# Optimization experiments

Hardware: AMD Instinct MI355X
Metric: run time of the kernel (lower is better)

Reference implementation:

```python
import jax, jax.numpy as jnp
import numpy as np

STRIDES = (8, 16, 32)
SIZES = ((80, 80), (40, 40), (20, 20))  # 640x640 input
PRE_TOP_K = 1000
KEEP_TOP_K = 100
IOU_THR = 0.65
SCORE_THR = 0.25
CLASS_OFFSET = 4096.0  # > max image extent, for class-aware NMS


def setup_inputs() -> dict:
    key = jax.random.key(0)
    ks = jax.random.split(key, 6)
    B, C = 8, 1203
    d = {}
    for i, (h, w) in enumerate(SIZES):
        d[f"cls_scores_{i}"] = jax.random.normal(ks[i], (B, C, h, w), dtype=jnp.float32)
        d[f"bbox_preds_{i}"] = jax.random.uniform(ks[3 + i], (B, 4, h, w), dtype=jnp.float32)
    return d


def _flatten(feats, ch):
    B = feats[0].shape[0]
    return jnp.concatenate([f.transpose(0, 2, 3, 1).reshape(B, -1, ch) for f in feats], axis=1)


def _priors():
    pts, strs = [], []
    for (h, w), s in zip(SIZES, STRIDES):
        yy, xx = jnp.meshgrid(jnp.arange(h, dtype=jnp.float32), jnp.arange(w, dtype=jnp.float32), indexing="ij")
        pts.append(jnp.stack([(xx.ravel() + 0.5) * s, (yy.ravel() + 0.5) * s], axis=-1))
        strs.append(jnp.full((h * w,), float(s), dtype=jnp.float32))
    return jnp.concatenate(pts, 0), jnp.concatenate(strs, 0)


def _decode(priors, preds, stride):
    # DistancePointBBoxCoder: preds are LTRB distances scaled by stride.
    d = preds * stride[None, :, None]  # [B,N,4]
    x1 = priors[None, :, 0] - d[..., 0]
    y1 = priors[None, :, 1] - d[..., 1]
    x2 = priors[None, :, 0] + d[..., 2]
    y2 = priors[None, :, 1] + d[..., 3]
    return jnp.stack([x1, y1, x2, y2], axis=-1)


def _iou_matrix(b):
    area = (b[:, 2] - b[:, 0]) * (b[:, 3] - b[:, 1])
    lt = jnp.maximum(b[:, None, :2], b[None, :, :2])
    rb = jnp.minimum(b[:, None, 2:], b[None, :, 2:])
    wh = jnp.clip(rb - lt, 0.0)
    inter = wh[..., 0] * wh[..., 1]
    return inter / (area[:, None] + area[None, :] - inter + 1e-7)


def _nms_single(boxes, scores, labels):
    # boxes [N,4], scores [N] (max over classes), labels [N] int
    ts, idx = jax.lax.top_k(scores, PRE_TOP_K)
    b = boxes[idx]
    l = labels[idx]
    valid = ts > SCORE_THR
    off = b + (l.astype(b.dtype) * CLASS_OFFSET)[:, None]  # class-aware trick
    iou = _iou_matrix(off)  # [K,K]

    def body(keep, i):
        suppressed = jnp.any(keep & (iou[:, i] > IOU_THR))
        keep = keep.at[i].set(valid[i] & ~suppressed)
        return keep, None

    keep, _ = jax.lax.scan(body, jnp.zeros((PRE_TOP_K,), bool), jnp.arange(PRE_TOP_K))
    kept_scores = jnp.where(keep, ts, -1.0)
    fs, fi = jax.lax.top_k(kept_scores, KEEP_TOP_K)
    m = fs > 0.0
    det_boxes = jnp.where(m[:, None], b[fi], 0.0)
    det_scores = jnp.where(m, fs, 0.0)
    det_labels = jnp.where(m, l[fi], -1)
    num_dets = m.sum().astype(jnp.int32)
    return num_dets, det_boxes, det_scores, det_labels


def reference(cls_scores_0, cls_scores_1, cls_scores_2, bbox_preds_0, bbox_preds_1, bbox_preds_2):
    C = cls_scores_0.shape[1]
    cls_scores = jax.nn.sigmoid(_flatten([cls_scores_0, cls_scores_1, cls_scores_2], C))  # [B,N,C]
    preds = _flatten([bbox_preds_0, bbox_preds_1, bbox_preds_2], 4)  # [B,N,4]
    priors, stride = _priors()
    boxes = _decode(priors, preds, stride)  # [B,N,4]
    max_scores = cls_scores.max(axis=-1)  # [B,N]
    labels = cls_scores.argmax(axis=-1)  # [B,N]
    num_dets, det_boxes, det_scores, det_labels = jax.vmap(_nms_single)(boxes, max_scores, labels)
    return num_dets, det_boxes, det_scores, det_labels
```

## Files before the change

kernel.cpp:

```cpp
#include <hip/hip_runtime.h>
#include <math.h>

#pragma clang fp contract(off)

typedef unsigned long long u64;
typedef unsigned int u32;
typedef float f4 __attribute__((ext_vector_type(4)));
typedef unsigned long long u64x2 __attribute__((ext_vector_type(2)));

#define BB 8
#define CC_TOT 1203
#define NANC 8400
#define NSEL 1000
#define NCAND 1024
#define NT 1024
#define NBATCH 128
#define NCHUNK_MAX 16

__device__ __forceinline__ u32 okey32(float v) {
  u32 b = __float_as_uint(v);
  return (b & 0x80000000u) ? ~b : (b | 0x80000000u);
}

__device__ __forceinline__ float unokey32(u32 ok) {
  u32 fb = (ok & 0x80000000u) ? (ok & 0x7FFFFFFFu) : ~ok;
  return __uint_as_float(fb);
}

__global__ __launch_bounds__(256) void kmax(const float* __restrict__ cls0,
                                            const float* __restrict__ cls1,
                                            const float* __restrict__ cls2,
                                            u64* __restrict__ part,
                                            int chunkSz, int nchunk) {
  int bx = blockIdx.x;
  int per = nchunk * BB;
  int tg = bx / per;
  int rem = bx - tg * per;
  int chunk = rem >> 3;
  int b = rem & 7;
  const float* cls; int hw4, aoff, col0;
  if (tg < 7)      { cls = cls0; hw4 = 1600; aoff = 0;    col0 = tg << 8; }
  else if (tg < 9) { cls = cls1; hw4 = 400;  aoff = 6400; col0 = (tg - 7) << 8; }
  else             { cls = cls2; hw4 = 100;  aoff = 8000; col0 = 0; }
  int col = col0 + (int)threadIdx.x;
  if (col >= hw4) return;
  int c0 = chunk * chunkSz;
  int c1 = c0 + chunkSz; if (c1 > CC_TOT) c1 = CC_TOT;

  const f4* base = (const f4*)cls + (size_t)b * CC_TOT * hw4 + col;
  f4 m = (f4){-3.4e38f, -3.4e38f, -3.4e38f, -3.4e38f};
  int ix0 = c0, ix1 = c0, ix2 = c0, ix3 = c0;

#define UPD(v, c)                                   \
  do {                                              \
    if ((v)[0] > m[0]) { m[0] = (v)[0]; ix0 = (c); } \
    if ((v)[1] > m[1]) { m[1] = (v)[1]; ix1 = (c); } \
    if ((v)[2] > m[2]) { m[2] = (v)[2]; ix2 = (c); } \
    if ((v)[3] > m[3]) { m[3] = (v)[3]; ix3 = (c); } \
  } while (0)

  int c = c0;
  for (; c + 8 <= c1; c += 8) {
    const f4* p = base + (size_t)c * hw4;
    f4 v0 = p[0];
    f4 v1 = p[(size_t)1 * hw4];
    f4 v2 = p[(size_t)2 * hw4];
    f4 v3 = p[(size_t)3 * hw4];
    f4 v4 = p[(size_t)4 * hw4];
    f4 v5 = p[(size_t)5 * hw4];
    f4 v6 = p[(size_t)6 * hw4];
    f4 v7 = p[(size_t)7 * hw4];
    UPD(v0, c + 0); UPD(v1, c + 1); UPD(v2, c + 2); UPD(v3, c + 3);
    UPD(v4, c + 4); UPD(v5, c + 5); UPD(v6, c + 6); UPD(v7, c + 7);
  }
  for (; c < c1; ++c) {
    f4 v = base[(size_t)c * hw4];
    UPD(v, c);
  }
#undef UPD

  u64* dst = part + ((size_t)chunk * BB + b) * NANC + aoff + (size_t)col * 4;
  u64x2 s01 = { ((u64)okey32(m[0]) << 32) | (u64)(u32)~(u32)ix0,
                ((u64)okey32(m[1]) << 32) | (u64)(u32)~(u32)ix1 };
  u64x2 s23 = { ((u64)okey32(m[2]) << 32) | (u64)(u32)~(u32)ix2,
                ((u64)okey32(m[3]) << 32) | (u64)(u32)~(u32)ix3 };
  *((u64x2*)dst)     = s01;
  *((u64x2*)dst + 1) = s23;
}

__global__ __launch_bounds__(256) void kreduce(const u64* __restrict__ part,
                                               u64* __restrict__ fin, int nchunk) {
  int a = blockIdx.x * 256 + threadIdx.x;
  if (a >= NANC) return;
  int b = blockIdx.y;
  size_t off = (size_t)b * NANC + a;
  const size_t PL = (size_t)BB * NANC;
  const u64* p = part + off;
  u64 m = p[0];
  int ch = 1;
  for (; ch + 4 <= nchunk; ch += 4) {
    u64 v0 = p[(size_t)(ch + 0) * PL];
    u64 v1 = p[(size_t)(ch + 1) * PL];
    u64 v2 = p[(size_t)(ch + 2) * PL];
    u64 v3 = p[(size_t)(ch + 3) * PL];
    u64 a01 = (v0 > v1) ? v0 : v1;
    u64 a23 = (v2 > v3) ? v2 : v3;
    u64 a03 = (a01 > a23) ? a01 : a23;
    m = (a03 > m) ? a03 : m;
  }
  for (; ch < nchunk; ++ch) {
    u64 v = p[(size_t)ch * PL];
    m = (v > m) ? v : m;
  }
  u32 lab = ~(u32)m;
  fin[off] = (m & 0xFFFFFFFF00000000ull) | ((u64)(u32)(0xFFFFu - (u32)a) << 16) | (u64)(lab & 0xFFFFu);
}

struct DecodeArrays {
  float xo1[NCAND], yo1[NCAND], xo2[NCAND], yo2[NCAND], ar[NCAND];
  float rx1[NCAND], ry1[NCAND], rx2[NCAND], ry2[NCAND], sc[NCAND];
  int lab[NCAND], val[NCAND];
};

__device__ __forceinline__ void hist_add_clustered(u32* hist, u32 digit, int lane) {
  u64 peers = ~0ull;
  for (int bit = 0; bit < 13; ++bit) {
    u64 bal = __ballot((digit >> bit) & 1u);
    peers &= ((digit >> bit) & 1u) ? bal : ~bal;
  }
  int leader = __ffsll((unsigned long long)peers) - 1;
  if (digit < 4096u && lane == leader)
    atomicAdd(&hist[digit], (u32)__popcll((unsigned long long)peers));
}

__device__ __forceinline__ void suffix_pick(u32* hist, u32* waveTot, u32* waveSufExcl,
                                            u64* prefixSh, u32* rankSh,
                                            u64 prefix, u32 rank, int shift,
                                            int tid, int lane, int wv) {
  u32 l0 = hist[4 * tid], l1 = hist[4 * tid + 1], l2 = hist[4 * tid + 2], l3 = hist[4 * tid + 3];
  u32 psum = l0 + l1 + l2 + l3;
  u32 x = psum;
  for (int s = 1; s < 64; s <<= 1) { u32 v = __shfl_down(x, s); if (lane + s < 64) x += v; }
  if (lane == 0) waveTot[wv] = x;
  __syncthreads();
  if (tid < 16) {
    u32 y = waveTot[tid]; u32 z = y;
    for (int s = 1; s < 16; s <<= 1) { u32 v = __shfl_down(z, s); if (tid + s < 16) z += v; }
    waveSufExcl[tid] = z - y;
  }
  __syncthreads();
  u32 S = x + waveSufExcl[wv];
  u32 G3 = S - psum; u32 G2 = G3 + l3; u32 G1 = G2 + l2; u32 G0 = G1 + l1;
  u32 r = rank;
  if      (G3 < r && G3 + l3 >= r) { *prefixSh = prefix | ((u64)(4u * tid + 3) << shift); *rankSh = r - G3; }
  else if (G2 < r && G2 + l2 >= r) { *prefixSh = prefix | ((u64)(4u * tid + 2) << shift); *rankSh = r - G2; }
  else if (G1 < r && G1 + l1 >= r) { *prefixSh = prefix | ((u64)(4u * tid + 1) << shift); *rankSh = r - G1; }
  else if (G0 < r && G0 + l0 >= r) { *prefixSh = prefix | ((u64)(4u * tid + 0) << shift); *rankSh = r - G0; }
}

__device__ __forceinline__ u64 radix_select(const u64* keys, int n, u32 target,
                                            u32* hist, u32* waveTot, u32* waveSufExcl,
                                            u64* prefixSh, u32* rankSh,
                                            int tid, int lane, int wv) {
  u64 prefix = 0; u32 rank = target;
  for (int pass = 3; pass >= 0; --pass) {
    int shift = 16 + pass * 12;
    for (int i = tid; i < 4096; i += NT) hist[i] = 0;
    __syncthreads();
    u64 hiMask = (pass == 3) ? 0ull : ((~0ull) << (shift + 12));
    if (pass == 3) {
      for (int i = tid; i < n; i += NT) {
        u64 k = keys[i];
        hist_add_clustered(hist, (u32)((k >> shift) & 4095u), lane);
      }
    } else {
      for (int i = tid; i < n; i += NT) {
        u64 k = keys[i];
        if ((k & hiMask) == (prefix & hiMask))
          atomicAdd(&hist[(u32)((k >> shift) & 4095u)], 1u);
      }
    }
    __syncthreads();
    suffix_pick(hist, waveTot, waveSufExcl, prefixSh, rankSh, prefix, rank, shift, tid, lane, wv);
    __syncthreads();
    prefix = *prefixSh; rank = *rankSh;
    __syncthreads();
  }
  return prefix;
}

__device__ __forceinline__ void gather_ge(const u64* keys, int n, u64 K, u64* dst, u32* cnt,
                                          int tid, int lane, u32 bound) {
  for (int i = tid; i < n; i += NT) {
    u64 k = keys[i];
    bool sel = (k >= K);
    u64 mask = __ballot(sel);
    if (mask) {
      int leader = __ffsll((unsigned long long)mask) - 1;
      u32 basep = 0;
      if (lane == leader) basep = atomicAdd(cnt, (u32)__popcll((unsigned long long)mask));
      basep = __shfl((int)basep, leader);
      if (sel) {
        u32 pos = basep + (u32)__popcll((unsigned long long)(mask & ((1ull << lane) - 1ull)));
        if (pos < bound) dst[pos] = k;
      }
    }
  }
}

__device__ __forceinline__ void decode_into(DecodeArrays* d, int rk, u64 my, int b,
                                            const float* bb0, const float* bb1, const float* bb2) {
  int label = (int)(u32)(my & 0xFFFFull);
  int idx = 0xFFFF - (int)(u32)((my >> 16) & 0xFFFFull);
  float logit = unokey32((u32)(my >> 32));
  float sc = 1.0f / (1.0f + expf(-logit));

  int w, str, off, hwl; const float* bb;
  if (idx < 6400)      { w = 80; str = 8;  off = 0;    hwl = 6400; bb = bb0; }
  else if (idx < 8000) { w = 40; str = 16; off = 6400; hwl = 1600; bb = bb1; }
  else                 { w = 20; str = 32; off = 8000; hwl = 400;  bb = bb2; }
  int p = idx - off;
  int y = p / w;
  int x = p - y * w;
  float fs = (float)str;
  float px = ((float)x + 0.5f) * fs;
  float py = ((float)y + 0.5f) * fs;
  const float* bp = bb + (size_t)b * 4 * hwl + p;
  float t0 = bp[0] * fs;
  float t1 = bp[hwl] * fs;
  float t2 = bp[2 * hwl] * fs;
  float t3 = bp[3 * hwl] * fs;
  float x1 = px - t0, y1 = py - t1, x2 = px + t2, y2 = py + t3;
  float lo = (float)label * 4096.0f;
  float ox1 = x1 + lo, oy1 = y1 + lo, ox2 = x2 + lo, oy2 = y2 + lo;
  float area = (ox2 - ox1) * (oy2 - oy1);

  d->xo1[rk] = ox1; d->yo1[rk] = oy1; d->xo2[rk] = ox2; d->yo2[rk] = oy2; d->ar[rk] = area;
  d->rx1[rk] = x1;  d->ry1[rk] = y1;  d->rx2[rk] = x2;  d->ry2[rk] = y2;  d->sc[rk] = sc;
  d->lab[rk] = label;
  d->val[rk] = (sc > 0.25f) ? 1 : 0;
}

__device__ __forceinline__ int nms_pass(const DecodeArrays* d, int bound, int lane, int* outIdx) {
  float ax1 = 0, ay1 = 0, ax2 = 0, ay2 = 0, aar = 0; int aon = 0;
  float bx1 = 0, by1 = 0, bx2 = 0, by2 = 0, bar = 0; int bon = 0;
  int kept = 0;
  for (int i = 0; i < bound; ++i) {
    if (kept >= 100) break;
    float cx1 = d->xo1[i], cy1 = d->yo1[i], cx2 = d->xo2[i], cy2 = d->yo2[i], car = d->ar[i];
    bool sup = false;
    if (aon) {
      float ltx = fmaxf(ax1, cx1), lty = fmaxf(ay1, cy1);
      float rbx = fminf(ax2, cx2), rby = fminf(ay2, cy2);
      float wd = fmaxf(rbx - ltx, 0.0f), ht = fmaxf(rby - lty, 0.0f);
      float inter = wd * ht;
      sup = sup || ((inter / (aar + car - inter + 1e-7f)) > 0.65f);
    }
    if (bon) {
      float ltx = fmaxf(bx1, cx1), lty = fmaxf(by1, cy1);
      float rbx = fminf(bx2, cx2), rby = fminf(by2, cy2);
      float wd = fmaxf(rbx - ltx, 0.0f), ht = fmaxf(rby - lty, 0.0f);
      float inter = wd * ht;
      sup = sup || ((inter / (bar + car - inter + 1e-7f)) > 0.65f);
    }
    bool anysup = __any(sup);
    if (d->val[i] != 0 && !anysup) {
      if (kept < 64) {
        if (lane == kept) { ax1 = cx1; ay1 = cy1; ax2 = cx2; ay2 = cy2; aar = car; aon = 1; }
      } else {
        if (lane == kept - 64) { bx1 = cx1; by1 = cy1; bx2 = cx2; by2 = cy2; bar = car; bon = 1; }
      }
      if (lane == 0) outIdx[kept] = i;
      ++kept;
    }
  }
  return kept;
}

__global__ __launch_bounds__(1024) void knms(const u64* __restrict__ fin,
                                             const float* __restrict__ bb0,
                                             const float* __restrict__ bb1,
                                             const float* __restrict__ bb2,
                                             float* __restrict__ out) {
  __shared__ union ShU {
    u64 fk[NANC];
    DecodeArrays d;
  } sh;
  __shared__ u32 hist[4096];
  __shared__ u32 waveTot[16];
  __shared__ u32 waveSufExcl[16];
  __shared__ u64 prefixSh;
  __shared__ u32 rankSh;
  __shared__ u32 gcnt, aCnt, cCnt;
  __shared__ __align__(16) u64 cand[NCAND];
  __shared__ __align__(16) u64 candA[NBATCH];
  __shared__ __align__(16) u32 cm[NBATCH * 4];
  __shared__ u64 VwSh[2];
  __shared__ int outIdx[128];
  __shared__ int keptSh;

  int b = blockIdx.x;
  int tid = threadIdx.x;
  int lane = tid & 63;
  int wv = tid >> 6;

  for (int i = tid; i < 4096; i += NT) hist[i] = 0;
  if (tid == 0) { aCnt = 0; cCnt = 0; }
  __syncthreads();
  {
    const u64x2* fsrc = (const u64x2*)(fin + (size_t)b * NANC);
    u64x2* fdst = (u64x2*)sh.fk;
    for (int i = tid; i < NANC / 2; i += NT) {
      u64x2 v = fsrc[i];
      fdst[i] = v;
      hist_add_clustered(hist, (u32)(v[0] >> 52), lane);
      hist_add_clustered(hist, (u32)(v[1] >> 52), lane);
    }
  }
  __syncthreads();

  suffix_pick(hist, waveTot, waveSufExcl, &prefixSh, &rankSh, 0ull, NBATCH, 52, tid, lane, wv);
  __syncthreads();
  u64 pfx3 = prefixSh; u32 r3 = rankSh;
  u32 d3 = (u32)(pfx3 >> 52);
  __syncthreads();

  for (int i = tid; i < NANC; i += NT) {
    u64 k = sh.fk[i];
    u32 dig = (u32)(k >> 52);
    bool selA = dig > d3;
    u64 mA = __ballot(selA);
    if (mA) {
      int leader = __ffsll((unsigned long long)mA) - 1;
      u32 basep = 0;
      if (lane == leader) basep = atomicAdd(&aCnt, (u32)__popcll((unsigned long long)mA));
      basep = __shfl((int)basep, leader);
      if (selA) {
        u32 pos = basep + (u32)__popcll((unsigned long long)(mA & ((1ull << lane) - 1ull)));
        if (pos < NBATCH) candA[pos] = k;
      }
    }
    bool selC = (dig == d3);
    u64 mC = __ballot(selC);
    if (mC) {
      int leader = __ffsll((unsigned long long)mC) - 1;
      u32 basep = 0;
      if (lane == leader) basep = atomicAdd(&cCnt, (u32)__popcll((unsigned long long)mC));
      basep = __shfl((int)basep, leader);
      if (selC) {
        u32 pos = basep + (u32)__popcll((unsigned long long)(mC & ((1ull << lane) - 1ull)));
        if (pos < NCAND) cand[pos] = k;
      }
    }
  }
  __syncthreads();

  u32 cnt3 = cCnt;
  if (cnt3 <= NCAND) {
    u64 pfx = pfx3; u32 rk = r3;
    for (int pass = 2; pass >= 0; --pass) {
      int shift = 16 + pass * 12;
      for (int i = tid; i < 4096; i += NT) hist[i] = 0;
      __syncthreads();
      u64 hiMask = (~0ull) << (shift + 12);
      for (int i = tid; i < (int)cnt3; i += NT) {
        u64 k = cand[i];
        if ((k & hiMask) == (pfx & hiMask))
          atomicAdd(&hist[(u32)((k >> shift) & 4095u)], 1u);
      }
      __syncthreads();
      suffix_pick(hist, waveTot, waveSufExcl, &prefixSh, &rankSh, pfx, rk, shift, tid, lane, wv);
      __syncthreads();
      pfx = prefixSh; rk = rankSh;
      __syncthreads();
    }
    u64 K2 = pfx;
    gather_ge(cand, (int)cnt3, K2, candA, &aCnt, tid, lane, NBATCH);
    __syncthreads();
  } else {
    if (tid == 0) aCnt = 0;
    __syncthreads();
    u64 K2 = radix_select(sh.fk, NANC, NBATCH, hist, waveTot, waveSufExcl,
                          &prefixSh, &rankSh, tid, lane, wv);
    gather_ge(sh.fk, NANC, K2, candA, &aCnt, tid, lane, NBATCH);
    __syncthreads();
  }

  if (tid < NBATCH) {
    u64 my = candA[tid];
    int rk = 0;
    const u64x2* cav = (const u64x2*)candA;
    #pragma unroll
    for (int j2 = 0; j2 < NBATCH / 2; ++j2) {
      u64x2 p = cav[j2];
      rk += (p[0] > my) ? 1 : 0;
      rk += (p[1] > my) ? 1 : 0;
    }
    decode_into(&sh.d, rk, my, b, bb0, bb1, bb2);
  }
  if (tid < NBATCH * 4) cm[tid] = 0;
  __syncthreads();

  if (tid < NBATCH) {
    u64 bal = __ballot(sh.d.val[tid] != 0);
    if (lane == 0) VwSh[tid >> 6] = bal;
  }

  {
    int c = tid & 127;
    int g = tid >> 7;
    float cx1 = sh.d.xo1[c], cy1 = sh.d.yo1[c], cx2 = sh.d.xo2[c], cy2 = sh.d.yo2[c], car = sh.d.ar[c];
    u32 bits = 0;
    int j0 = g * 16;
    for (int jj = 0; jj < 16; ++jj) {
      int j = j0 + jj;
      float ltx = fmaxf(sh.d.xo1[j], cx1), lty = fmaxf(sh.d.yo1[j], cy1);
      float rbx = fminf(sh.d.xo2[j], cx2), rby = fminf(sh.d.yo2[j], cy2);
      float wd = fmaxf(rbx - ltx, 0.0f), ht = fmaxf(rby - lty, 0.0f);
      float inter = wd * ht;
      bool sup = (inter / (sh.d.ar[j] + car - inter + 1e-7f)) > 0.65f;
      bits |= sup ? (1u << jj) : 0u;
    }
    atomicOr(&cm[c * 4 + (g >> 1)], bits << ((g & 1) * 16));
  }
  __syncthreads();

  if (tid == 0) {
    u32 K0 = 0, K1 = 0, K2w = 0, K3 = 0;
    u64 V0 = VwSh[0], V1 = VwSh[1];
    int kept = 0;
    for (int i = 0; i < NBATCH && kept < 100; ++i) {
      const u32* c4 = &cm[i * 4];
      u32 sup = (c4[0] & K0) | (c4[1] & K1) | (c4[2] & K2w) | (c4[3] & K3);
      bool valid = (((i < 64) ? (V0 >> i) : (V1 >> (i - 64))) & 1ull) != 0ull;
      if (valid && sup == 0u) {
        if (i < 32) K0 |= 1u << i;
        else if (i < 64) K1 |= 1u << (i - 32);
        else if (i < 96) K2w |= 1u << (i - 64);
        else K3 |= 1u << (i - 96);
        outIdx[kept++] = i;
      }
    }
    keptSh = kept;
  }
  __syncthreads();

  if (keptSh < 100) {
    {
      const u64x2* fsrc = (const u64x2*)(fin + (size_t)b * NANC);
      u64x2* fdst = (u64x2*)sh.fk;
      for (int i = tid; i < NANC / 2; i += NT) fdst[i] = fsrc[i];
    }
    __syncthreads();
    u64 K = radix_select(sh.fk, NANC, NSEL, hist, waveTot, waveSufExcl,
                         &prefixSh, &rankSh, tid, lane, wv);
    if (tid == 0) gcnt = 0;
    __syncthreads();
    gather_ge(sh.fk, NANC, K, cand, &gcnt, tid, lane, NSEL);
    __syncthreads();
    if (tid < NSEL) {
      u64 my = cand[tid];
      int rk = 0;
      const u64x2* cbv = (const u64x2*)cand;
      for (int j2 = 0; j2 < NSEL / 2; ++j2) {
        u64x2 p = cbv[j2];
        rk += (p[0] > my) ? 1 : 0;
        rk += (p[1] > my) ? 1 : 0;
      }
      decode_into(&sh.d, rk, my, b, bb0, bb1, bb2);
    }
    __syncthreads();
    if (tid < 64) {
      int kept = nms_pass(&sh.d, NSEL, lane, outIdx);
      if (lane == 0) keptSh = kept;
    }
    __syncthreads();
  }

  int kept = keptSh;
  float* o_nd = out;
  float* o_box = out + BB;
  float* o_sc = out + BB + BB * 100 * 4;
  float* o_lb = out + BB + BB * 100 * 4 + BB * 100;
  if (tid == 0) o_nd[b] = (float)kept;
  if (tid < 100) {
    int s = tid;
    float v0 = 0, v1 = 0, v2 = 0, v3 = 0, sv = 0, lv = -1.0f;
    if (s < kept) {
      int i = outIdx[s];
      v0 = sh.d.rx1[i]; v1 = sh.d.ry1[i]; v2 = sh.d.rx2[i]; v3 = sh.d.ry2[i];
      sv = sh.d.sc[i]; lv = (float)sh.d.lab[i];
    }
    float* bo = o_box + ((size_t)b * 100 + s) * 4;
    bo[0] = v0; bo[1] = v1; bo[2] = v2; bo[3] = v3;
    o_sc[b * 100 + s] = sv;
    o_lb[b * 100 + s] = lv;
  }
}

extern "C" void kernel_launch(void* const* d_in, const int* in_sizes, int n_in,
                              void* d_out, int out_size, void* d_ws, size_t ws_size,
                              hipStream_t stream) {
  const float* cls0 = (const float*)d_in[0];
  const float* bb0  = (const float*)d_in[1];
  const float* cls1 = (const float*)d_in[2];
  const float* bb1  = (const float*)d_in[3];
  const float* cls2 = (const float*)d_in[4];
  const float* bb2  = (const float*)d_in[5];

  size_t planeB = (size_t)BB * NANC * sizeof(u64);
  u64* fin = (u64*)d_ws;
  u64* part;
  int nchunk;
  if (ws_size >= 2 * planeB) {
    size_t avail = (ws_size - planeB) / planeB;
    nchunk = (int)(avail < NCHUNK_MAX ? avail : NCHUNK_MAX);
    part = fin + (size_t)BB * NANC;
  } else {
    nchunk = 1;
    part = fin;
  }
  int chunkSz = (CC_TOT + nchunk - 1) / nchunk;
  nchunk = (CC_TOT + chunkSz - 1) / chunkSz;

  kmax<<<dim3(10 * nchunk * BB), dim3(256), 0, stream>>>(cls0, cls1, cls2, part, chunkSz, nchunk);
  kreduce<<<dim3((NANC + 255) / 256, BB), dim3(256), 0, stream>>>(part, fin, nchunk);
  knms<<<dim3(BB), dim3(NT), 0, stream>>>(fin, bb0, bb1, bb2, (float*)d_out);
}
```

Before: 120.7 us.

## Fuse chunk reduction into NMS kernel and shortcut radix selection

Removes the separate kreduce launch and has the NMS kernel reduce the per-chunk partial max keys directly while building the first histogram. This drops one kernel launch and the round trip through the fin buffer. It also adds an early exit from the radix select when the chosen bin holds exactly the remaining rank, and replaces the greedy 128-candidate keep loop with a find-first-set walk over a live mask. The cost is that only 8 blocks now do the chunk reduction, and they do it again in the fallback path.

```diff
diff --git a/kernel.cpp b/kernel.cpp
--- a/kernel.cpp
+++ b/kernel.cpp
@@ -88,40 +88,37 @@
   *((u64x2*)dst + 1) = s23;
 }
 
-__global__ __launch_bounds__(256) void kreduce(const u64* __restrict__ part,
-                                               u64* __restrict__ fin, int nchunk) {
-  int a = blockIdx.x * 256 + threadIdx.x;
-  if (a >= NANC) return;
-  int b = blockIdx.y;
-  size_t off = (size_t)b * NANC + a;
-  const size_t PL = (size_t)BB * NANC;
-  const u64* p = part + off;
-  u64 m = p[0];
-  int ch = 1;
-  for (; ch + 4 <= nchunk; ch += 4) {
-    u64 v0 = p[(size_t)(ch + 0) * PL];
-    u64 v1 = p[(size_t)(ch + 1) * PL];
-    u64 v2 = p[(size_t)(ch + 2) * PL];
-    u64 v3 = p[(size_t)(ch + 3) * PL];
-    u64 a01 = (v0 > v1) ? v0 : v1;
-    u64 a23 = (v2 > v3) ? v2 : v3;
-    u64 a03 = (a01 > a23) ? a01 : a23;
-    m = (a03 > m) ? a03 : m;
-  }
-  for (; ch < nchunk; ++ch) {
-    u64 v = p[(size_t)ch * PL];
-    m = (v > m) ? v : m;
-  }
-  u32 lab = ~(u32)m;
-  fin[off] = (m & 0xFFFFFFFF00000000ull) | ((u64)(u32)(0xFFFFu - (u32)a) << 16) | (u64)(lab & 0xFFFFu);
-}
-
 struct DecodeArrays {
   float xo1[NCAND], yo1[NCAND], xo2[NCAND], yo2[NCAND], ar[NCAND];
   float rx1[NCAND], ry1[NCAND], rx2[NCAND], ry2[NCAND], sc[NCAND];
   int lab[NCAND], val[NCAND];
 };
 
+__device__ __forceinline__ u64x2 reduce_pair(const u64x2* psrc, size_t PL2, int nchunk, int i) {
+  u64x2 m = psrc[i];
+  for (int ch = 1; ch < nchunk; ++ch) {
+    u64x2 v = psrc[(size_t)ch * PL2 + i];
+    if (v[0] > m[0]) m[0] = v[0];
+    if (v[1] > m[1]) m[1] = v[1];
+  }
+  u32 i0 = (u32)(2 * i), i1 = (u32)(2 * i + 1);
+  u64x2 r;
+  r[0] = (m[0] & 0xFFFFFFFF00000000ull) | ((u64)(0xFFFFu - i0) << 16) | (u64)(~(u32)m[0] & 0xFFFFu);
+  r[1] = (m[1] & 0xFFFFFFFF00000000ull) | ((u64)(0xFFFFu - i1) << 16) | (u64)(~(u32)m[1] & 0xFFFFu);
+  return r;
+}
+
+__device__ __forceinline__ void hist_add12(u32* hist, u32 digit, int lane) {
+  u64 peers = ~0ull;
+  for (int bit = 0; bit < 12; ++bit) {
+    u64 bal = __ballot((digit >> bit) & 1u);
+    peers &= ((digit >> bit) & 1u) ? bal : ~bal;
+  }
+  int leader = __ffsll((unsigned long long)peers) - 1;
+  if (lane == leader)
+    atomicAdd(&hist[digit], (u32)__popcll((unsigned long long)peers));
+}
+
 __device__ __forceinline__ void hist_add_clustered(u32* hist, u32 digit, int lane) {
   u64 peers = ~0ull;
   for (int bit = 0; bit < 13; ++bit) {
@@ -134,7 +131,7 @@
 }
 
 __device__ __forceinline__ void suffix_pick(u32* hist, u32* waveTot, u32* waveSufExcl,
-                                            u64* prefixSh, u32* rankSh,
+                                            u64* prefixSh, u32* rankSh, u32* binCntSh,
                                             u64 prefix, u32 rank, int shift,
                                             int tid, int lane, int wv) {
   u32 l0 = hist[4 * tid], l1 = hist[4 * tid + 1], l2 = hist[4 * tid + 2], l3 = hist[4 * tid + 3];
@@ -152,15 +149,15 @@
   u32 S = x + waveSufExcl[wv];
   u32 G3 = S - psum; u32 G2 = G3 + l3; u32 G1 = G2 + l2; u32 G0 = G1 + l1;
   u32 r = rank;
-  if      (G3 < r && G3 + l3 >= r) { *prefixSh = prefix | ((u64)(4u * tid + 3) << shift); *rankSh = r - G3; }
-  else if (G2 < r && G2 + l2 >= r) { *prefixSh = prefix | ((u64)(4u * tid + 2) << shift); *rankSh = r - G2; }
-  else if (G1 < r && G1 + l1 >= r) { *prefixSh = prefix | ((u64)(4u * tid + 1) << shift); *rankSh = r - G1; }
-  else if (G0 < r && G0 + l0 >= r) { *prefixSh = prefix | ((u64)(4u * tid + 0) << shift); *rankSh = r - G0; }
+  if      (G3 < r && G3 + l3 >= r) { *prefixSh = prefix | ((u64)(4u * tid + 3) << shift); *rankSh = r - G3; *binCntSh = l3; }
+  else if (G2 < r && G2 + l2 >= r) { *prefixSh = prefix | ((u64)(4u * tid + 2) << shift); *rankSh = r - G2; *binCntSh = l2; }
+  else if (G1 < r && G1 + l1 >= r) { *prefixSh = prefix | ((u64)(4u * tid + 1) << shift); *rankSh = r - G1; *binCntSh = l1; }
+  else if (G0 < r && G0 + l0 >= r) { *prefixSh = prefix | ((u64)(4u * tid + 0) << shift); *rankSh = r - G0; *binCntSh = l0; }
 }
 
 __device__ __forceinline__ u64 radix_select(const u64* keys, int n, u32 target,
                                             u32* hist, u32* waveTot, u32* waveSufExcl,
-                                            u64* prefixSh, u32* rankSh,
+                                            u64* prefixSh, u32* rankSh, u32* binCntSh,
                                             int tid, int lane, int wv) {
   u64 prefix = 0; u32 rank = target;
   for (int pass = 3; pass >= 0; --pass) {
@@ -181,7 +178,7 @@
       }
     }
     __syncthreads();
-    suffix_pick(hist, waveTot, waveSufExcl, prefixSh, rankSh, prefix, rank, shift, tid, lane, wv);
+    suffix_pick(hist, waveTot, waveSufExcl, prefixSh, rankSh, binCntSh, prefix, rank, shift, tid, lane, wv);
     __syncthreads();
     prefix = *prefixSh; rank = *rankSh;
     __syncthreads();
@@ -277,7 +274,7 @@
   return kept;
 }
 
-__global__ __launch_bounds__(1024) void knms(const u64* __restrict__ fin,
+__global__ __launch_bounds__(1024) void knms(const u64* __restrict__ part, int nchunk,
                                              const float* __restrict__ bb0,
                                              const float* __restrict__ bb1,
                                              const float* __restrict__ bb2,
@@ -290,7 +287,7 @@
   __shared__ u32 waveTot[16];
   __shared__ u32 waveSufExcl[16];
   __shared__ u64 prefixSh;
-  __shared__ u32 rankSh;
+  __shared__ u32 rankSh, binCntSh;
   __shared__ u32 gcnt, aCnt, cCnt;
   __shared__ __align__(16) u64 cand[NCAND];
   __shared__ __align__(16) u64 candA[NBATCH];
@@ -304,84 +301,100 @@
   int lane = tid & 63;
   int wv = tid >> 6;
 
+  const u64x2* psrc = (const u64x2*)(part + (size_t)b * NANC);
+  const size_t PL2 = (size_t)BB * NANC / 2;
+
   for (int i = tid; i < 4096; i += NT) hist[i] = 0;
   if (tid == 0) { aCnt = 0; cCnt = 0; }
   __syncthreads();
   {
-    const u64x2* fsrc = (const u64x2*)(fin + (size_t)b * NANC);
     u64x2* fdst = (u64x2*)sh.fk;
     for (int i = tid; i < NANC / 2; i += NT) {
-      u64x2 v = fsrc[i];
-      fdst[i] = v;
-      hist_add_clustered(hist, (u32)(v[0] >> 52), lane);
-      hist_add_clustered(hist, (u32)(v[1] >> 52), lane);
-    }
-  }
-  __syncthreads();
-
-  suffix_pick(hist, waveTot, waveSufExcl, &prefixSh, &rankSh, 0ull, NBATCH, 52, tid, lane, wv);
-  __syncthreads();
-  u64 pfx3 = prefixSh; u32 r3 = rankSh;
+      u64x2 k = reduce_pair(psrc, PL2, nchunk, i);
+      fdst[i] = k;
+      hist_add12(hist, (u32)(k[0] >> 52), lane);
+      hist_add12(hist, (u32)(k[1] >> 52), lane);
+    }
+  }
+  __syncthreads();
+
+  suffix_pick(hist, waveTot, waveSufExcl, &prefixSh, &rankSh, &binCntSh,
+              0ull, NBATCH, 52, tid, lane, wv);
+  __syncthreads();
+  u64 pfx3 = prefixSh; u32 r3 = rankSh; u32 l3 = binCntSh;
   u32 d3 = (u32)(pfx3 >> 52);
   __syncthreads();
 
-  for (int i = tid; i < NANC; i += NT) {
-    u64 k = sh.fk[i];
-    u32 dig = (u32)(k >> 52);
-    bool selA = dig > d3;
-    u64 mA = __ballot(selA);
-    if (mA) {
-      int leader = __ffsll((unsigned long long)mA) - 1;
-      u32 basep = 0;
-      if (lane == leader) basep = atomicAdd(&aCnt, (u32)__popcll((unsigned long long)mA));
-      basep = __shfl((int)basep, leader);
-      if (selA) {
-        u32 pos = basep + (u32)__popcll((unsigned long long)(mA & ((1ull << lane) - 1ull)));
-        if (pos < NBATCH) candA[pos] = k;
-      }
-    }
-    bool selC = (dig == d3);
-    u64 mC = __ballot(selC);
-    if (mC) {
-      int leader = __ffsll((unsigned long long)mC) - 1;
-      u32 basep = 0;
-      if (lane == leader) basep = atomicAdd(&cCnt, (u32)__popcll((unsigned long long)mC));
-      basep = __shfl((int)basep, leader);
-      if (selC) {
-        u32 pos = basep + (u32)__popcll((unsigned long long)(mC & ((1ull << lane) - 1ull)));
-        if (pos < NCAND) cand[pos] = k;
-      }
-    }
-  }
-  __syncthreads();
-
-  u32 cnt3 = cCnt;
-  if (cnt3 <= NCAND) {
-    u64 pfx = pfx3; u32 rk = r3;
-    for (int pass = 2; pass >= 0; --pass) {
-      int shift = 16 + pass * 12;
-      for (int i = tid; i < 4096; i += NT) hist[i] = 0;
+  bool pathological = false;
+  if (l3 == r3) {
+    gather_ge(sh.fk, NANC, pfx3, candA, &aCnt, tid, lane, NBATCH);
+    __syncthreads();
+  } else {
+    for (int i = tid; i < NANC; i += NT) {
+      u64 k = sh.fk[i];
+      u32 dig = (u32)(k >> 52);
+      bool selA = dig > d3;
+      u64 mA = __ballot(selA);
+      if (mA) {
+        int leader = __ffsll((unsigned long long)mA) - 1;
+        u32 basep = 0;
+        if (lane == leader) basep = atomicAdd(&aCnt, (u32)__popcll((unsigned long long)mA));
+        basep = __shfl((int)basep, leader);
+        if (selA) {
+          u32 pos = basep + (u32)__popcll((unsigned long long)(mA & ((1ull << lane) - 1ull)));
+          if (pos < NBATCH) candA[pos] = k;
+        }
+      }
+      bool selC = (dig == d3);
+      u64 mC = __ballot(selC);
+      if (mC) {
+        int leader = __ffsll((unsigned long long)mC) - 1;
+        u32 basep = 0;
+        if (lane == leader) basep = atomicAdd(&cCnt, (u32)__popcll((unsigned long long)mC));
+        basep = __shfl((int)basep, leader);
+        if (selC) {
+          u32 pos = basep + (u32)__popcll((unsigned long long)(mC & ((1ull << lane) - 1ull)));
+          if (pos < NCAND) cand[pos] = k;
+        }
+      }
+    }
+    __syncthreads();
+
+    u32 cnt3 = cCnt;
+    if (cnt3 <= NCAND) {
+      u64 pfx = pfx3; u32 rk = r3;
+      u64 Kf = 0; bool done = false;
+      for (int pass = 2; pass >= 0 && !done; --pass) {
+        int shift = 16 + pass * 12;
+        for (int i = tid; i < 4096; i += NT) hist[i] = 0;
+        __syncthreads();
+        u64 hiMask = (~0ull) << (shift + 12);
+        for (int i = tid; i < (int)cnt3; i += NT) {
+          u64 k = cand[i];
+          if ((k & hiMask) == (pfx & hiMask))
+            atomicAdd(&hist[(u32)((k >> shift) & 4095u)], 1u);
+        }
+        __syncthreads();
+        suffix_pick(hist, waveTot, waveSufExcl, &prefixSh, &rankSh, &binCntSh,
+                    pfx, rk, shift, tid, lane, wv);
+        __syncthreads();
+        pfx = prefixSh; rk = rankSh;
+        u32 lc = binCntSh;
+        __syncthreads();
+        if (lc == rk || pass == 0) { done = true; Kf = pfx; }
+      }
+      gather_ge(cand, (int)cnt3, Kf, candA, &aCnt, tid, lane, NBATCH);
       __syncthreads();
-      u64 hiMask = (~0ull) << (shift + 12);
-      for (int i = tid; i < (int)cnt3; i += NT) {
-        u64 k = cand[i];
-        if ((k & hiMask) == (pfx & hiMask))
-          atomicAdd(&hist[(u32)((k >> shift) & 4095u)], 1u);
-      }
-      __syncthreads();
-      suffix_pick(hist, waveTot, waveSufExcl, &prefixSh, &rankSh, pfx, rk, shift, tid, lane, wv);
-      __syncthreads();
-      pfx = prefixSh; rk = rankSh;
-      __syncthreads();
-    }
-    u64 K2 = pfx;
-    gather_ge(cand, (int)cnt3, K2, candA, &aCnt, tid, lane, NBATCH);
-    __syncthreads();
-  } else {
+    } else {
+      pathological = true;
+    }
+  }
+
+  if (pathological) {
     if (tid == 0) aCnt = 0;
     __syncthreads();
     u64 K2 = radix_select(sh.fk, NANC, NBATCH, hist, waveTot, waveSufExcl,
-                          &prefixSh, &rankSh, tid, lane, wv);
+                          &prefixSh, &rankSh, &binCntSh, tid, lane, wv);
     gather_ge(sh.fk, NANC, K2, candA, &aCnt, tid, lane, NBATCH);
     __syncthreads();
   }
@@ -426,20 +439,23 @@
   __syncthreads();
 
   if (tid == 0) {
-    u32 K0 = 0, K1 = 0, K2w = 0, K3 = 0;
-    u64 V0 = VwSh[0], V1 = VwSh[1];
+    u32 L0 = (u32)VwSh[0], L1 = (u32)(VwSh[0] >> 32);
+    u32 L2 = (u32)VwSh[1], L3 = (u32)(VwSh[1] >> 32);
     int kept = 0;
-    for (int i = 0; i < NBATCH && kept < 100; ++i) {
+    while (kept < 100) {
+      int i;
+      if (L0)      i = __ffs(L0) - 1;
+      else if (L1) i = 31 + __ffs(L1);
+      else if (L2) i = 63 + __ffs(L2);
+      else if (L3) i = 95 + __ffs(L3);
+      else break;
+      outIdx[kept++] = i;
       const u32* c4 = &cm[i * 4];
-      u32 sup = (c4[0] & K0) | (c4[1] & K1) | (c4[2] & K2w) | (c4[3] & K3);
-      bool valid = (((i < 64) ? (V0 >> i) : (V1 >> (i - 64))) & 1ull) != 0ull;
-      if (valid && sup == 0u) {
-        if (i < 32) K0 |= 1u << i;
-        else if (i < 64) K1 |= 1u << (i - 32);
-        else if (i < 96) K2w |= 1u << (i - 64);
-        else K3 |= 1u << (i - 96);
-        outIdx[kept++] = i;
-      }
+      L0 &= ~c4[0]; L1 &= ~c4[1]; L2 &= ~c4[2]; L3 &= ~c4[3];
+      if (i < 32)      L0 &= ~(1u << i);
+      else if (i < 64) L1 &= ~(1u << (i - 32));
+      else if (i < 96) L2 &= ~(1u << (i - 64));
+      else             L3 &= ~(1u << (i - 96));
     }
     keptSh = kept;
   }
@@ -447,13 +463,13 @@
 
   if (keptSh < 100) {
     {
-      const u64x2* fsrc = (const u64x2*)(fin + (size_t)b * NANC);
       u64x2* fdst = (u64x2*)sh.fk;
-      for (int i = tid; i < NANC / 2; i += NT) fdst[i] = fsrc[i];
+      for (int i = tid; i < NANC / 2; i += NT)
+        fdst[i] = reduce_pair(psrc, PL2, nchunk, i);
     }
     __syncthreads();
     u64 K = radix_select(sh.fk, NANC, NSEL, hist, waveTot, waveSufExcl,
-                         &prefixSh, &rankSh, tid, lane, wv);
+                         &prefixSh, &rankSh, &binCntSh, tid, lane, wv);
     if (tid == 0) gcnt = 0;
     __syncthreads();
     gather_ge(sh.fk, NANC, K, cand, &gcnt, tid, lane, NSEL);
@@ -509,21 +525,13 @@
   const float* bb2  = (const float*)d_in[5];
 
   size_t planeB = (size_t)BB * NANC * sizeof(u64);
-  u64* fin = (u64*)d_ws;
-  u64* part;
-  int nchunk;
-  if (ws_size >= 2 * planeB) {
-    size_t avail = (ws_size - planeB) / planeB;
-    nchunk = (int)(avail < NCHUNK_MAX ? avail : NCHUNK_MAX);
-    part = fin + (size_t)BB * NANC;
-  } else {
-    nchunk = 1;
-    part = fin;
-  }
+  u64* part = (u64*)d_ws;
+  int nchunk = (int)(ws_size / planeB);
+  if (nchunk < 1) nchunk = 1;
+  if (nchunk > NCHUNK_MAX) nchunk = NCHUNK_MAX;
   int chunkSz = (CC_TOT + nchunk - 1) / nchunk;
   nchunk = (CC_TOT + chunkSz - 1) / chunkSz;
 
   kmax<<<dim3(10 * nchunk * BB), dim3(256), 0, stream>>>(cls0, cls1, cls2, part, chunkSz, nchunk);
-  kreduce<<<dim3((NANC + 255) / 256, BB), dim3(256), 0, stream>>>(part, fin, nchunk);
-  knms<<<dim3(BB), dim3(NT), 0, stream>>>(fin, bb0, bb1, bb2, (float*)d_out);
-}
+  knms<<<dim3(BB), dim3(NT), 0, stream>>>(part, nchunk, bb0, bb1, bb2, (float*)d_out);
+}
```

New measurement: 132.6 us. 9.9% more time.
